# Kernel optimization log

Hardware: AMD Instinct MI355X
Metric: run time of the kernel (lower is better)

Reference implementation:

```python
import math
import jax, jax.numpy as jnp
import numpy as np

B, S, D_IN = 4, 4096, 2048
HID, NH, HD, K = 256, 16, 128, 4
EPS = 1e-12  # F.normalize eps


def setup_inputs() -> dict:
    key = jax.random.key(0)
    k1, k2, k3, k4, k5 = jax.random.split(key, 5)
    bound = 1.0 / D_IN
    b_bound = 1.0 / math.sqrt(D_IN)
    return {
        "x": jax.random.normal(k1, (B, S, D_IN), dtype=jnp.float32),
        "router_w": jax.random.normal(k2, (HID, D_IN), dtype=jnp.float32) * (1.0 / math.sqrt(D_IN)),
        "head_centroids": jax.random.normal(k3, (NH, HID), dtype=jnp.float32),
        "temperature": jnp.zeros((1,), dtype=jnp.float32),
        "weight": jax.random.uniform(k4, (NH * HD, D_IN), minval=-bound, maxval=bound, dtype=jnp.float32),
        "bias": jax.random.uniform(k5, (NH * HD,), minval=-b_bound, maxval=b_bound, dtype=jnp.float32),
    }


def _l2norm(v, axis=-1):
    n = jnp.sqrt(jnp.sum(v * v, axis=axis, keepdims=True))
    return v / jnp.maximum(n, EPS)


def reference(x, router_w, head_centroids, temperature, weight, bias):
    # --- routing weights (eval mode: dropout = identity) ---
    z = jnp.einsum("bsd,hd->bsh", x, router_w)            # [B,S,HID]
    z_norm = _l2norm(z)                                     # [B,S,HID]
    c_norm = _l2norm(head_centroids)                        # [NH,HID]
    logits = jnp.einsum("bsh,nh->bsn", z_norm, c_norm)     # [B,S,NH]
    logits = logits / math.sqrt(HID) * jnp.exp(temperature[0])
    probs = jax.nn.softmax(logits, axis=-1)                 # [B,S,NH]

    # --- top-k head selection ---
    top_k_probs, top_k_indices = jax.lax.top_k(probs, K)    # [B,S,K]

    # --- dense linear over all heads, then gather selected heads ---
    full = jnp.einsum("bsd,od->bso", x, weight) + bias      # [B,S,NH*HD]
    full = full.reshape(B, S, NH, HD)
    selected = jnp.take_along_axis(full, top_k_indices[..., None], axis=2)  # [B,S,K,HD]
    selected = selected * top_k_probs[..., None]            # multiply_by_gates=True
    return selected.reshape(B, S, K * HD)
```

## Files before the change

### kernel.cpp

```cpp
#include <hip/hip_runtime.h>
#include <hip/hip_fp16.h>
#include <cstdint>
#include <cstddef>
#include <cmath>

#define T_TOK 16384
#define DIN   2048
#define HIDN  256
#define NHEAD 16
#define HDIM  128
#define NKT   32

typedef __attribute__((ext_vector_type(4))) float    f32x4;
typedef __attribute__((ext_vector_type(4))) int      i32x4;
typedef __attribute__((ext_vector_type(8))) _Float16 f16x8;
typedef __attribute__((ext_vector_type(4))) _Float16 f16x4;

#define OFF_XH   ((size_t)0)
#define OFF_XL   ((size_t)67108864)
#define OFF_WH   ((size_t)134217728)
#define OFF_RWH  ((size_t)142606336)
#define OFF_RWL  ((size_t)143654912)
#define OFF_CN   ((size_t)144703488)
#define OFF_GIDX ((size_t)144719872)
#define OFF_GPRB ((size_t)144982016)

__device__ __forceinline__ void gl_lds16(const void* g, void* l) {
  __builtin_amdgcn_global_load_lds(
      (const __attribute__((address_space(1))) unsigned int*)g,
      (__attribute__((address_space(3))) unsigned int*)l, 16, 0, 0);
}

__global__ void prep_convert(const float* __restrict__ x,
                             const float* __restrict__ w,
                             const float* __restrict__ rw,
                             _Float16* __restrict__ xh, _Float16* __restrict__ xl,
                             _Float16* __restrict__ wh,
                             _Float16* __restrict__ rwh, _Float16* __restrict__ rwl) {
  size_t i = (size_t)blockIdx.x * 256 + threadIdx.x;
  if (i < 8388608) {
    const f32x4 v = ((const f32x4*)x)[i];
    size_t t = i >> 9;
    int r4 = (int)(i & 511);
    int kt = r4 >> 4;
    int k  = (r4 & 15) << 2;
    size_t o = (((size_t)kt * T_TOK + t) << 6) + k;
    _Float16 h0 = (_Float16)v.x, h1 = (_Float16)v.y,
             h2 = (_Float16)v.z, h3 = (_Float16)v.w;
    *(f16x4*)(xh + o) = (f16x4){h0, h1, h2, h3};
    _Float16 l0 = (_Float16)((v.x - (float)h0) * 4096.0f);
    _Float16 l1 = (_Float16)((v.y - (float)h1) * 4096.0f);
    _Float16 l2 = (_Float16)((v.z - (float)h2) * 4096.0f);
    _Float16 l3 = (_Float16)((v.w - (float)h3) * 4096.0f);
    *(f16x4*)(xl + o) = (f16x4){l0, l1, l2, l3};
  } else if (i < 9437184) {
    size_t j = i - 8388608;
    const f32x4 v = ((const f32x4*)w)[j];
    size_t row = j >> 9;
    int r4 = (int)(j & 511);
    int kt = r4 >> 4;
    int k  = (r4 & 15) << 2;
    size_t o = (((size_t)kt * 2048 + row) << 6) + k;
    *(f16x4*)(wh + o) = (f16x4){(_Float16)(v.x * 64.0f), (_Float16)(v.y * 64.0f),
                                (_Float16)(v.z * 64.0f), (_Float16)(v.w * 64.0f)};
  } else if (i < 9568256) {
    size_t j = i - 9437184;
    const f32x4 v = ((const f32x4*)rw)[j];
    size_t row = j >> 9;
    int r4 = (int)(j & 511);
    int kt = r4 >> 4;
    int k  = (r4 & 15) << 2;
    size_t o = (((size_t)kt * 256 + row) << 6) + k;
    _Float16 h0 = (_Float16)v.x, h1 = (_Float16)v.y,
             h2 = (_Float16)v.z, h3 = (_Float16)v.w;
    *(f16x4*)(rwh + o) = (f16x4){h0, h1, h2, h3};
    _Float16 l0 = (_Float16)((v.x - (float)h0) * 4096.0f);
    _Float16 l1 = (_Float16)((v.y - (float)h1) * 4096.0f);
    _Float16 l2 = (_Float16)((v.z - (float)h2) * 4096.0f);
    _Float16 l3 = (_Float16)((v.w - (float)h3) * 4096.0f);
    *(f16x4*)(rwl + o) = (f16x4){l0, l1, l2, l3};
  }
}

__global__ void prep_cnorm(const float* __restrict__ c, float* __restrict__ cn) {
  int tid = threadIdx.x;
  int h = tid >> 4, j = tid & 15;
  double s = 0.0;
  #pragma unroll
  for (int q = 0; q < 16; q++) {
    double v = (double)c[h * HIDN + j * 16 + q];
    s = fma(v, v, s);
  }
  s += __shfl_xor(s, 1, 64);
  s += __shfl_xor(s, 2, 64);
  s += __shfl_xor(s, 4, 64);
  s += __shfl_xor(s, 8, 64);
  float nf = (float)fmax(sqrt(s), 1e-12);
  #pragma unroll
  for (int q = 0; q < 16; q++)
    cn[h * HIDN + j * 16 + q] = c[h * HIDN + j * 16 + q] / nf;
}

__launch_bounds__(512, 2)
__global__ void router_kernel(const _Float16* __restrict__ xh,
                              const _Float16* __restrict__ xl,
                              const _Float16* __restrict__ rwh,
                              const _Float16* __restrict__ rwl,
                              float* __restrict__ zf) {
  __shared__ struct { _Float16 Ah[64 * 64]; _Float16 Al[64 * 64]; _Float16 Bb[256 * 64]; } u;

  const int tid  = threadIdx.x;
  const int w    = tid >> 6;
  const int lane = tid & 63;
  const int lm   = lane & 15;
  const int quad = lane >> 4;
  const int wm   = w & 1;
  const int wn   = w >> 1;
  const int t0   = blockIdx.x * 64;

  double zacc[2][4][4];
  f32x4 accB[2][4];
  #pragma unroll
  for (int a = 0; a < 2; a++)
    #pragma unroll
    for (int b = 0; b < 4; b++) {
      accB[a][b] = (f32x4)0.0f;
      #pragma unroll
      for (int q = 0; q < 4; q++) zacc[a][b][q] = 0.0;
    }

  for (int kt = 0; kt < NKT; kt++) {
    if (kt) __syncthreads();
    {
      const char* ah_src = (const char*)(xh + (((size_t)kt * T_TOK + t0) << 6));
      const char* al_src = (const char*)(xl + (((size_t)kt * T_TOK + t0) << 6));
      const char* bh_src = (const char*)(rwh + (((size_t)kt * 256) << 6));
      gl_lds16(ah_src + w * 1024 + lane * 16, (char*)u.Ah + w * 1024);
      gl_lds16(al_src + w * 1024 + lane * 16, (char*)u.Al + w * 1024);
      #pragma unroll
      for (int c = 0; c < 4; c++)
        gl_lds16(bh_src + (w * 4 + c) * 1024 + lane * 16, (char*)u.Bb + (w * 4 + c) * 1024);
    }
    __syncthreads();
    f32x4 accA[2][4];
    #pragma unroll
    for (int a = 0; a < 2; a++)
      #pragma unroll
      for (int b = 0; b < 4; b++) accA[a][b] = (f32x4)0.0f;
    #pragma unroll
    for (int ks = 0; ks < 2; ks++) {
      const int ko = ks * 32 + quad * 8;
      f16x8 ah[2], al[2], bh[4];
      #pragma unroll
      for (int fm = 0; fm < 2; fm++) {
        int r = wm * 32 + fm * 16 + lm;
        ah[fm] = *(const f16x8*)(u.Ah + r * 64 + ko);
        al[fm] = *(const f16x8*)(u.Al + r * 64 + ko);
      }
      #pragma unroll
      for (int fn = 0; fn < 4; fn++) {
        int r = wn * 64 + fn * 16 + lm;
        bh[fn] = *(const f16x8*)(u.Bb + r * 64 + ko);
      }
      #pragma unroll
      for (int fm = 0; fm < 2; fm++)
        #pragma unroll
        for (int fn = 0; fn < 4; fn++) {
          accA[fm][fn] = __builtin_amdgcn_mfma_f32_16x16x32_f16(ah[fm], bh[fn], accA[fm][fn], 0, 0, 0);
          accB[fm][fn] = __builtin_amdgcn_mfma_f32_16x16x32_f16(al[fm], bh[fn], accB[fm][fn], 0, 0, 0);
        }
    }
    __syncthreads();
    {
      const char* bl_src = (const char*)(rwl + (((size_t)kt * 256) << 6));
      #pragma unroll
      for (int c = 0; c < 4; c++)
        gl_lds16(bl_src + (w * 4 + c) * 1024 + lane * 16, (char*)u.Bb + (w * 4 + c) * 1024);
    }
    __syncthreads();
    #pragma unroll
    for (int ks = 0; ks < 2; ks++) {
      const int ko = ks * 32 + quad * 8;
      f16x8 ah[2], bl[4];
      #pragma unroll
      for (int fm = 0; fm < 2; fm++) {
        int r = wm * 32 + fm * 16 + lm;
        ah[fm] = *(const f16x8*)(u.Ah + r * 64 + ko);
      }
      #pragma unroll
      for (int fn = 0; fn < 4; fn++) {
        int r = wn * 64 + fn * 16 + lm;
        bl[fn] = *(const f16x8*)(u.Bb + r * 64 + ko);
      }
      #pragma unroll
      for (int fm = 0; fm < 2; fm++)
        #pragma unroll
        for (int fn = 0; fn < 4; fn++)
          accB[fm][fn] = __builtin_amdgcn_mfma_f32_16x16x32_f16(ah[fm], bl[fn], accB[fm][fn], 0, 0, 0);
    }
    #pragma unroll
    for (int fm = 0; fm < 2; fm++)
      #pragma unroll
      for (int fn = 0; fn < 4; fn++)
        #pragma unroll
        for (int q = 0; q < 4; q++)
          zacc[fm][fn][q] += (double)accA[fm][fn][q];
  }

  #pragma unroll
  for (int fm = 0; fm < 2; fm++)
    #pragma unroll
    for (int fn = 0; fn < 4; fn++)
      #pragma unroll
      for (int i2 = 0; i2 < 4; i2++) {
        const int row = t0 + wm * 32 + fm * 16 + quad * 4 + i2;
        const int col = wn * 64 + fn * 16 + lm;
        zf[(size_t)row * 256 + col] =
            (float)(zacc[fm][fn][i2] + (double)accB[fm][fn][i2] * (1.0 / 4096.0));
      }
}

__launch_bounds__(256, 4)
__global__ void route_topk(const float* __restrict__ zf,
                           const float* __restrict__ cn,
                           const float* __restrict__ temp,
                           int* __restrict__ gidx,
                           float* __restrict__ gprb) {
  const int tid  = threadIdx.x;
  const int w    = tid >> 6;
  const int lane = tid & 63;
  const int lm   = lane & 15;
  const int quad = lane >> 4;
  const int t    = blockIdx.x * 16 + w * 4 + quad;

  const float* zrow = zf + (size_t)t * 256;
  double ssq = 0.0;
  #pragma unroll
  for (int c16 = 0; c16 < 16; c16++) {
    double zv = (double)zrow[c16 * 16 + lm];
    ssq = fma(zv, zv, ssq);
  }
  ssq += __shfl_xor(ssq, 1, 64);
  ssq += __shfl_xor(ssq, 2, 64);
  ssq += __shfl_xor(ssq, 4, 64);
  ssq += __shfl_xor(ssq, 8, 64);
  const float* crow = cn + lm * 256;
  double dot = 0.0;
  #pragma unroll 8
  for (int c = 0; c < 256; c++)
    dot = fma((double)zrow[c], (double)crow[c], dot);
  double nd = fmax(sqrt(ssq), 1e-12);
  float lgt = (float)(dot / nd) * 0.0625f * expf(temp[0]);

  float mx = lgt;
  mx = fmaxf(mx, __shfl_xor(mx, 1, 64));
  mx = fmaxf(mx, __shfl_xor(mx, 2, 64));
  mx = fmaxf(mx, __shfl_xor(mx, 4, 64));
  mx = fmaxf(mx, __shfl_xor(mx, 8, 64));
  float e = (float)exp((double)(lgt - mx));
  float s = e;
  s = s + __shfl_xor(s, 8, 64);
  s = s + __shfl_xor(s, 1, 64);
  s = s + __shfl_xor(s, 2, 64);
  s = s + __shfl_xor(s, 4, 64);
  float p = e / s;

  float pc = p;
  int bi[4]; float bp[4];
  #pragma unroll
  for (int k = 0; k < 4; k++) {
    float bv = pc; int bh = lm;
    #pragma unroll
    for (int m = 1; m < 16; m <<= 1) {
      float ov = __shfl_xor(bv, m, 64);
      int   oh = __shfl_xor(bh, m, 64);
      bool take = (ov > bv) || (ov == bv && oh < bh);
      bv = take ? ov : bv;
      bh = take ? oh : bh;
    }
    bi[k] = bh; bp[k] = bv;
    if (lm == bh) pc = -1.0f;
  }
  if (lm == 0) {
    *(i32x4*)(gidx + (size_t)t * 4) = (i32x4){bi[0], bi[1], bi[2], bi[3]};
    *(f32x4*)(gprb + (size_t)t * 4) = (f32x4){bp[0], bp[1], bp[2], bp[3]};
  }
}

__launch_bounds__(256, 2)
__global__ void main_gemm(const _Float16* __restrict__ xh,
                          const _Float16* __restrict__ wh,
                          const float* __restrict__ bias,
                          const int* __restrict__ gidx,
                          const float* __restrict__ gprb,
                          float* __restrict__ out) {
  __shared__ _Float16 As[128 * 64];
  __shared__ _Float16 Bs[128 * 64];
  __shared__ int   slot[128];
  __shared__ float scl[128];

  const int tid  = threadIdx.x;
  const int w    = tid >> 6;
  const int lane = tid & 63;
  const int lm   = lane & 15;
  const int quad = lane >> 4;
  const int wm   = w & 1;
  const int wn   = w >> 1;
  const int t0   = blockIdx.x * 128;
  const int h    = blockIdx.y;

  if (tid < 128) {
    i32x4 g = *(const i32x4*)(gidx + (size_t)(t0 + tid) * 4);
    f32x4 p = *(const f32x4*)(gprb + (size_t)(t0 + tid) * 4);
    int s = -1; float sc = 0.f;
    if      (g.x == h) { s = 0; sc = p.x; }
    else if (g.y == h) { s = 1; sc = p.y; }
    else if (g.z == h) { s = 2; sc = p.z; }
    else if (g.w == h) { s = 3; sc = p.w; }
    slot[tid] = s; scl[tid] = sc;
  }

  f32x4 acc[4][4];
  #pragma unroll
  for (int a = 0; a < 4; a++)
    #pragma unroll
    for (int b = 0; b < 4; b++) acc[a][b] = (f32x4)0.0f;

  for (int kt = 0; kt < NKT; kt++) {
    if (kt) __syncthreads();
    const char* asrc = (const char*)(xh + (((size_t)kt * T_TOK + t0) << 6));
    const char* bsrc = (const char*)(wh + (((size_t)kt * 2048 + h * 128) << 6));
    #pragma unroll
    for (int c = 0; c < 4; c++) {
      gl_lds16(asrc + (w * 4 + c) * 1024 + lane * 16, (char*)As + (w * 4 + c) * 1024);
      gl_lds16(bsrc + (w * 4 + c) * 1024 + lane * 16, (char*)Bs + (w * 4 + c) * 1024);
    }
    __syncthreads();
    #pragma unroll
    for (int ks = 0; ks < 2; ks++) {
      const int ko = ks * 32 + quad * 8;
      f16x8 a[4], b[4];
      #pragma unroll
      for (int f = 0; f < 4; f++)
        a[f] = *(const f16x8*)(As + (wm * 64 + f * 16 + lm) * 64 + ko);
      #pragma unroll
      for (int f = 0; f < 4; f++)
        b[f] = *(const f16x8*)(Bs + (wn * 64 + f * 16 + lm) * 64 + ko);
      #pragma unroll
      for (int fm = 0; fm < 4; fm++)
        #pragma unroll
        for (int fn = 0; fn < 4; fn++)
          acc[fm][fn] = __builtin_amdgcn_mfma_f32_16x16x32_f16(a[fm], b[fn], acc[fm][fn], 0, 0, 0);
    }
  }

  float bias_v[4];
  #pragma unroll
  for (int fn = 0; fn < 4; fn++)
    bias_v[fn] = bias[h * 128 + wn * 64 + fn * 16 + lm];

  #pragma unroll
  for (int fm = 0; fm < 4; fm++) {
    const int rbase = wm * 64 + fm * 16 + quad * 4;
    #pragma unroll
    for (int i2 = 0; i2 < 4; i2++) {
      const int rr = rbase + i2;
      const int s = slot[rr];
      if (s >= 0) {
        const float sc = scl[rr];
        const size_t base = (size_t)(t0 + rr) * 512 + (size_t)s * 128 + wn * 64;
        #pragma unroll
        for (int fn = 0; fn < 4; fn++)
          out[base + fn * 16 + lm] = (acc[fm][fn][i2] * (1.0f / 64.0f) + bias_v[fn]) * sc;
      }
    }
  }
}

extern "C" void kernel_launch(void* const* d_in, const int* in_sizes, int n_in,
                              void* d_out, int out_size, void* d_ws, size_t ws_size,
                              hipStream_t stream) {
  const float* x    = (const float*)d_in[0];
  const float* rw   = (const float*)d_in[1];
  const float* hc   = (const float*)d_in[2];
  const float* temp = (const float*)d_in[3];
  const float* wt   = (const float*)d_in[4];
  const float* bias = (const float*)d_in[5];
  float* out = (float*)d_out;
  char* ws = (char*)d_ws;

  _Float16* xh   = (_Float16*)(ws + OFF_XH);
  _Float16* xl   = (_Float16*)(ws + OFF_XL);
  _Float16* wh   = (_Float16*)(ws + OFF_WH);
  _Float16* rwh  = (_Float16*)(ws + OFF_RWH);
  _Float16* rwl  = (_Float16*)(ws + OFF_RWL);
  float*    cn   = (float*)(ws + OFF_CN);
  int*      gidx = (int*)(ws + OFF_GIDX);
  float*    gprb = (float*)(ws + OFF_GPRB);
  float*    zf   = out;

  hipLaunchKernelGGL(prep_convert, dim3(37376), dim3(256), 0, stream,
                     x, wt, rw, xh, xl, wh, rwh, rwl);
  hipLaunchKernelGGL(prep_cnorm, dim3(1), dim3(256), 0, stream, hc, cn);
  hipLaunchKernelGGL(router_kernel, dim3(256), dim3(512), 0, stream,
                     xh, xl, rwh, rwl, zf);
  hipLaunchKernelGGL(route_topk, dim3(1024), dim3(256), 0, stream,
                     zf, cn, temp, gidx, gprb);
  hipLaunchKernelGGL(main_gemm, dim3(128, 16), dim3(256), 0, stream,
                     xh, wh, bias, gidx, gprb, out);
}
```

Baseline: 529.9 us.

## Replace dense per-head GEMM with routed sparse GEMM over gathered tokens

The top-k kernel now builds per-head token lists with atomic counters (a permutation plus gate probabilities), and a new sparse GEMM gathers only the tokens routed to each head. Before, every head was computed for all tokens, so this cuts that matmul work to roughly K/NH of the dense cost. The router GEMM is also split across two column blocks, each holding both hi and lo weight halves in LDS, which removes the mid-iteration reload and barriers. The risk is a fixed per-head capacity of 4608: if routing is imbalanced, tokens past the cap are dropped and their output slots are never written.

```diff
diff --git a/kernel.cpp b/kernel.cpp
--- a/kernel.cpp
+++ b/kernel.cpp
@@ -10,6 +10,7 @@
 #define NHEAD 16
 #define HDIM  128
 #define NKT   32
+#define CAPH  4608
 
 typedef __attribute__((ext_vector_type(4))) float    f32x4;
 typedef __attribute__((ext_vector_type(4))) int      i32x4;
@@ -22,8 +23,9 @@
 #define OFF_RWH  ((size_t)142606336)
 #define OFF_RWL  ((size_t)143654912)
 #define OFF_CN   ((size_t)144703488)
-#define OFF_GIDX ((size_t)144719872)
-#define OFF_GPRB ((size_t)144982016)
+#define OFF_CNT  (OFF_XL)
+#define OFF_PERM (OFF_XL + 1024)
+#define OFF_PR   (OFF_PERM + (size_t)NHEAD * CAPH * 4)
 
 __device__ __forceinline__ void gl_lds16(const void* g, void* l) {
   __builtin_amdgcn_global_load_lds(
@@ -107,7 +109,12 @@
                               const _Float16* __restrict__ rwh,
                               const _Float16* __restrict__ rwl,
                               float* __restrict__ zf) {
-  __shared__ struct { _Float16 Ah[64 * 64]; _Float16 Al[64 * 64]; _Float16 Bb[256 * 64]; } u;
+  __shared__ struct {
+    _Float16 Ah[64 * 64];
+    _Float16 Al[64 * 64];
+    _Float16 Bh[128 * 64];
+    _Float16 Bl[128 * 64];
+  } u;
 
   const int tid  = threadIdx.x;
   const int w    = tid >> 6;
@@ -117,13 +124,14 @@
   const int wm   = w & 1;
   const int wn   = w >> 1;
   const int t0   = blockIdx.x * 64;
-
-  double zacc[2][4][4];
-  f32x4 accB[2][4];
+  const int nb   = blockIdx.y;
+
+  double zacc[2][2][4];
+  f32x4 accB[2][2];
   #pragma unroll
   for (int a = 0; a < 2; a++)
     #pragma unroll
-    for (int b = 0; b < 4; b++) {
+    for (int b = 0; b < 2; b++) {
       accB[a][b] = (f32x4)0.0f;
       #pragma unroll
       for (int q = 0; q < 4; q++) zacc[a][b][q] = 0.0;
@@ -134,23 +142,26 @@
     {
       const char* ah_src = (const char*)(xh + (((size_t)kt * T_TOK + t0) << 6));
       const char* al_src = (const char*)(xl + (((size_t)kt * T_TOK + t0) << 6));
-      const char* bh_src = (const char*)(rwh + (((size_t)kt * 256) << 6));
+      const char* bh_src = (const char*)(rwh + (((size_t)kt * 256 + nb * 128) << 6));
+      const char* bl_src = (const char*)(rwl + (((size_t)kt * 256 + nb * 128) << 6));
       gl_lds16(ah_src + w * 1024 + lane * 16, (char*)u.Ah + w * 1024);
       gl_lds16(al_src + w * 1024 + lane * 16, (char*)u.Al + w * 1024);
       #pragma unroll
-      for (int c = 0; c < 4; c++)
-        gl_lds16(bh_src + (w * 4 + c) * 1024 + lane * 16, (char*)u.Bb + (w * 4 + c) * 1024);
+      for (int c = 0; c < 2; c++) {
+        gl_lds16(bh_src + (w * 2 + c) * 1024 + lane * 16, (char*)u.Bh + (w * 2 + c) * 1024);
+        gl_lds16(bl_src + (w * 2 + c) * 1024 + lane * 16, (char*)u.Bl + (w * 2 + c) * 1024);
+      }
     }
     __syncthreads();
-    f32x4 accA[2][4];
+    f32x4 accA[2][2];
     #pragma unroll
     for (int a = 0; a < 2; a++)
       #pragma unroll
-      for (int b = 0; b < 4; b++) accA[a][b] = (f32x4)0.0f;
+      for (int b = 0; b < 2; b++) accA[a][b] = (f32x4)0.0f;
     #pragma unroll
     for (int ks = 0; ks < 2; ks++) {
       const int ko = ks * 32 + quad * 8;
-      f16x8 ah[2], al[2], bh[4];
+      f16x8 ah[2], al[2], bh[2];
       #pragma unroll
       for (int fm = 0; fm < 2; fm++) {
         int r = wm * 32 + fm * 16 + lm;
@@ -158,50 +169,42 @@
         al[fm] = *(const f16x8*)(u.Al + r * 64 + ko);
       }
       #pragma unroll
-      for (int fn = 0; fn < 4; fn++) {
-        int r = wn * 64 + fn * 16 + lm;
-        bh[fn] = *(const f16x8*)(u.Bb + r * 64 + ko);
+      for (int fn = 0; fn < 2; fn++) {
+        int r = wn * 32 + fn * 16 + lm;
+        bh[fn] = *(const f16x8*)(u.Bh + r * 64 + ko);
       }
       #pragma unroll
       for (int fm = 0; fm < 2; fm++)
         #pragma unroll
-        for (int fn = 0; fn < 4; fn++) {
+        for (int fn = 0; fn < 2; fn++) {
           accA[fm][fn] = __builtin_amdgcn_mfma_f32_16x16x32_f16(ah[fm], bh[fn], accA[fm][fn], 0, 0, 0);
           accB[fm][fn] = __builtin_amdgcn_mfma_f32_16x16x32_f16(al[fm], bh[fn], accB[fm][fn], 0, 0, 0);
         }
     }
-    __syncthreads();
-    {
-      const char* bl_src = (const char*)(rwl + (((size_t)kt * 256) << 6));
-      #pragma unroll
-      for (int c = 0; c < 4; c++)
-        gl_lds16(bl_src + (w * 4 + c) * 1024 + lane * 16, (char*)u.Bb + (w * 4 + c) * 1024);
-    }
-    __syncthreads();
     #pragma unroll
     for (int ks = 0; ks < 2; ks++) {
       const int ko = ks * 32 + quad * 8;
-      f16x8 ah[2], bl[4];
+      f16x8 ah[2], bl[2];
       #pragma unroll
       for (int fm = 0; fm < 2; fm++) {
         int r = wm * 32 + fm * 16 + lm;
         ah[fm] = *(const f16x8*)(u.Ah + r * 64 + ko);
       }
       #pragma unroll
-      for (int fn = 0; fn < 4; fn++) {
-        int r = wn * 64 + fn * 16 + lm;
-        bl[fn] = *(const f16x8*)(u.Bb + r * 64 + ko);
+      for (int fn = 0; fn < 2; fn++) {
+        int r = wn * 32 + fn * 16 + lm;
+        bl[fn] = *(const f16x8*)(u.Bl + r * 64 + ko);
       }
       #pragma unroll
       for (int fm = 0; fm < 2; fm++)
         #pragma unroll
-        for (int fn = 0; fn < 4; fn++)
+        for (int fn = 0; fn < 2; fn++)
           accB[fm][fn] = __builtin_amdgcn_mfma_f32_16x16x32_f16(ah[fm], bl[fn], accB[fm][fn], 0, 0, 0);
     }
     #pragma unroll
     for (int fm = 0; fm < 2; fm++)
       #pragma unroll
-      for (int fn = 0; fn < 4; fn++)
+      for (int fn = 0; fn < 2; fn++)
         #pragma unroll
         for (int q = 0; q < 4; q++)
           zacc[fm][fn][q] += (double)accA[fm][fn][q];
@@ -210,22 +213,27 @@
   #pragma unroll
   for (int fm = 0; fm < 2; fm++)
     #pragma unroll
-    for (int fn = 0; fn < 4; fn++)
+    for (int fn = 0; fn < 2; fn++)
       #pragma unroll
       for (int i2 = 0; i2 < 4; i2++) {
         const int row = t0 + wm * 32 + fm * 16 + quad * 4 + i2;
-        const int col = wn * 64 + fn * 16 + lm;
+        const int col = nb * 128 + wn * 32 + fn * 16 + lm;
         zf[(size_t)row * 256 + col] =
             (float)(zacc[fm][fn][i2] + (double)accB[fm][fn][i2] * (1.0 / 4096.0));
       }
+}
+
+__global__ void zero_cnt(int* __restrict__ cnt) {
+  if (threadIdx.x < NHEAD) cnt[threadIdx.x] = 0;
 }
 
 __launch_bounds__(256, 4)
 __global__ void route_topk(const float* __restrict__ zf,
                            const float* __restrict__ cn,
                            const float* __restrict__ temp,
-                           int* __restrict__ gidx,
-                           float* __restrict__ gprb) {
+                           int* __restrict__ cnt,
+                           int* __restrict__ perm,
+                           float* __restrict__ pr) {
   const int tid  = threadIdx.x;
   const int w    = tid >> 6;
   const int lane = tid & 63;
@@ -282,22 +290,32 @@
     if (lm == bh) pc = -1.0f;
   }
   if (lm == 0) {
-    *(i32x4*)(gidx + (size_t)t * 4) = (i32x4){bi[0], bi[1], bi[2], bi[3]};
-    *(f32x4*)(gprb + (size_t)t * 4) = (f32x4){bp[0], bp[1], bp[2], bp[3]};
-  }
-}
-
-__launch_bounds__(256, 2)
-__global__ void main_gemm(const _Float16* __restrict__ xh,
-                          const _Float16* __restrict__ wh,
-                          const float* __restrict__ bias,
-                          const int* __restrict__ gidx,
-                          const float* __restrict__ gprb,
-                          float* __restrict__ out) {
+    #pragma unroll
+    for (int k = 0; k < 4; k++) {
+      int hs = bi[k];
+      int pos = atomicAdd(&cnt[hs], 1);
+      if (pos < CAPH) {
+        perm[hs * CAPH + pos] = (t << 2) | k;
+        pr[hs * CAPH + pos]   = bp[k];
+      }
+    }
+  }
+}
+
+__launch_bounds__(256, 4)
+__global__ void main_sparse(const _Float16* __restrict__ xh,
+                            const _Float16* __restrict__ wh,
+                            const float* __restrict__ bias,
+                            const int* __restrict__ cnt,
+                            const int* __restrict__ perm,
+                            const float* __restrict__ pr,
+                            float* __restrict__ out) {
   __shared__ _Float16 As[128 * 64];
   __shared__ _Float16 Bs[128 * 64];
-  __shared__ int   slot[128];
-  __shared__ float scl[128];
+  __shared__ int   tokS[128];
+  __shared__ int   slotS[128];
+  __shared__ float prbS[128];
+  __shared__ int   vldS[128];
 
   const int tid  = threadIdx.x;
   const int w    = tid >> 6;
@@ -306,19 +324,27 @@
   const int quad = lane >> 4;
   const int wm   = w & 1;
   const int wn   = w >> 1;
-  const int t0   = blockIdx.x * 128;
   const int h    = blockIdx.y;
 
+  const int cnt_h = min(cnt[h], CAPH);
+  const int base  = blockIdx.x * 128;
+  if (base >= cnt_h) return;
+  const int rows = min(128, cnt_h - base);
+
   if (tid < 128) {
-    i32x4 g = *(const i32x4*)(gidx + (size_t)(t0 + tid) * 4);
-    f32x4 p = *(const f32x4*)(gprb + (size_t)(t0 + tid) * 4);
-    int s = -1; float sc = 0.f;
-    if      (g.x == h) { s = 0; sc = p.x; }
-    else if (g.y == h) { s = 1; sc = p.y; }
-    else if (g.z == h) { s = 2; sc = p.z; }
-    else if (g.w == h) { s = 3; sc = p.w; }
-    slot[tid] = s; scl[tid] = sc;
-  }
+    int idx = h * CAPH + base + (tid < rows ? tid : 0);
+    int e = perm[idx];
+    tokS[tid]  = e >> 2;
+    slotS[tid] = e & 3;
+    prbS[tid]  = pr[idx];
+    vldS[tid]  = (tid < rows) ? 1 : 0;
+  }
+  __syncthreads();
+
+  int tokc[4];
+  #pragma unroll
+  for (int c = 0; c < 4; c++)
+    tokc[c] = tokS[w * 32 + c * 8 + (lane >> 3)];
 
   f32x4 acc[4][4];
   #pragma unroll
@@ -326,13 +352,14 @@
     #pragma unroll
     for (int b = 0; b < 4; b++) acc[a][b] = (f32x4)0.0f;
 
+  const char* xh_b = (const char*)xh;
   for (int kt = 0; kt < NKT; kt++) {
     if (kt) __syncthreads();
-    const char* asrc = (const char*)(xh + (((size_t)kt * T_TOK + t0) << 6));
     const char* bsrc = (const char*)(wh + (((size_t)kt * 2048 + h * 128) << 6));
     #pragma unroll
     for (int c = 0; c < 4; c++) {
-      gl_lds16(asrc + (w * 4 + c) * 1024 + lane * 16, (char*)As + (w * 4 + c) * 1024);
+      gl_lds16(xh_b + (((size_t)kt * T_TOK + tokc[c]) << 7) + (lane & 7) * 16,
+               (char*)As + (w * 4 + c) * 1024);
       gl_lds16(bsrc + (w * 4 + c) * 1024 + lane * 16, (char*)Bs + (w * 4 + c) * 1024);
     }
     __syncthreads();
@@ -365,13 +392,12 @@
     #pragma unroll
     for (int i2 = 0; i2 < 4; i2++) {
       const int rr = rbase + i2;
-      const int s = slot[rr];
-      if (s >= 0) {
-        const float sc = scl[rr];
-        const size_t base = (size_t)(t0 + rr) * 512 + (size_t)s * 128 + wn * 64;
+      if (vldS[rr]) {
+        const float sc = prbS[rr];
+        const size_t obase = (size_t)tokS[rr] * 512 + (size_t)slotS[rr] * 128 + wn * 64;
         #pragma unroll
         for (int fn = 0; fn < 4; fn++)
-          out[base + fn * 16 + lm] = (acc[fm][fn][i2] * (1.0f / 64.0f) + bias_v[fn]) * sc;
+          out[obase + fn * 16 + lm] = (acc[fm][fn][i2] * (1.0f / 64.0f) + bias_v[fn]) * sc;
       }
     }
   }
@@ -395,17 +421,19 @@
   _Float16* rwh  = (_Float16*)(ws + OFF_RWH);
   _Float16* rwl  = (_Float16*)(ws + OFF_RWL);
   float*    cn   = (float*)(ws + OFF_CN);
-  int*      gidx = (int*)(ws + OFF_GIDX);
-  float*    gprb = (float*)(ws + OFF_GPRB);
+  int*      cnt  = (int*)(ws + OFF_CNT);
+  int*      perm = (int*)(ws + OFF_PERM);
+  float*    pr   = (float*)(ws + OFF_PR);
   float*    zf   = out;
 
   hipLaunchKernelGGL(prep_convert, dim3(37376), dim3(256), 0, stream,
                      x, wt, rw, xh, xl, wh, rwh, rwl);
   hipLaunchKernelGGL(prep_cnorm, dim3(1), dim3(256), 0, stream, hc, cn);
-  hipLaunchKernelGGL(router_kernel, dim3(256), dim3(512), 0, stream,
+  hipLaunchKernelGGL(router_kernel, dim3(256, 2), dim3(512), 0, stream,
                      xh, xl, rwh, rwl, zf);
+  hipLaunchKernelGGL(zero_cnt, dim3(1), dim3(64), 0, stream, cnt);
   hipLaunchKernelGGL(route_topk, dim3(1024), dim3(256), 0, stream,
-                     zf, cn, temp, gidx, gprb);
-  hipLaunchKernelGGL(main_gemm, dim3(128, 16), dim3(256), 0, stream,
-                     xh, wh, bias, gidx, gprb, out);
-}
+                     zf, cn, temp, cnt, perm, pr);
+  hipLaunchKernelGGL(main_sparse, dim3(36, 16), dim3(256), 0, stream,
+                     xh, wh, bias, cnt, perm, pr, out);
+}
```

Measured after the change: 683.7 us. 1.29x slower.
